# Kernel tuning notes

Measured on AMD Instinct MI355X. Metric: run time of the kernel, lower is better.

## Reference

```python
import jax, jax.numpy as jnp
import numpy as np

B, N, D, H = 2, 2048, 384, 8
Dh = D // H          # 48
G = Dh // 3          # 16 3-vectors per head
EPS = 1e-5


def setup_inputs() -> dict:
    key = jax.random.key(0)
    ks = jax.random.split(key, 8)
    x = jax.random.normal(ks[0], (B, N, D), dtype=jnp.float32)
    # per-node SE(3) frames: proper rotation matrices via QR of random Gaussians
    raw = jax.random.normal(ks[1], (B, N, 3, 3), dtype=jnp.float32)
    q, r = jnp.linalg.qr(raw)
    sign = jnp.sign(jnp.diagonal(r, axis1=-2, axis2=-1))
    frames = q * sign[..., None, :]
    s = 1.0 / np.sqrt(D)
    Wq = jax.random.normal(ks[2], (D, D), dtype=jnp.float32) * s
    Wk = jax.random.normal(ks[3], (D, D), dtype=jnp.float32) * s
    Wv = jax.random.normal(ks[4], (D, D), dtype=jnp.float32) * s
    Wo = jax.random.normal(ks[5], (D, D), dtype=jnp.float32) * s
    bo = jnp.zeros((D,), dtype=jnp.float32)
    gamma = jnp.ones((D,), dtype=jnp.float32)
    beta = jnp.zeros((D,), dtype=jnp.float32)
    return {"x": x, "frames": frames, "Wq": Wq, "Wk": Wk, "Wv": Wv,
            "Wo": Wo, "bo": bo, "gamma": gamma, "beta": beta}


def _rotate(frames, t):
    # t: [B,N,H,Dh] -> rotate each 3-vector chunk by the node's frame R_i
    b, n, h, dh = t.shape
    t3 = t.reshape(b, n, h, dh // 3, 3)
    r3 = jnp.einsum('bnij,bnhgj->bnhgi', frames, t3)
    return r3.reshape(b, n, h, dh)


def reference(x, frames, Wq, Wk, Wv, Wo, bo, gamma, beta):
    b, n, d = x.shape
    Q = (x @ Wq.T).reshape(b, n, H, Dh)
    K = (x @ Wk.T).reshape(b, n, H, Dh)
    V = (x @ Wv.T).reshape(b, n, H, Dh)
    # SE(3) frame-conditioned attention: rotate Q,K into each node's local frame
    Qr = _rotate(frames, Q)
    Kr = _rotate(frames, K)
    scores = jnp.einsum('bqhd,bkhd->bhqk', Qr, Kr) / np.sqrt(Dh)
    attn = jax.nn.softmax(scores, axis=-1)
    out = jnp.einsum('bhqk,bkhd->bqhd', attn, V).reshape(b, n, d)
    out = out @ Wo.T + bo          # out_proj; dropout is identity in eval
    y = x + out                     # residual
    mu = jnp.mean(y, axis=-1, keepdims=True)
    var = jnp.var(y, axis=-1, keepdims=True)
    return (y - mu) * jax.lax.rsqrt(var + EPS) * gamma + beta
```

## Files before the change

### kernel.cpp

```cpp
#include <hip/hip_runtime.h>
#include <hip/hip_bf16.h>
#include <math.h>

constexpr int B = 2, N = 2048, D = 384, H = 8, Dh = 48;
constexpr int M = B * N;
constexpr float EPS = 1e-5f;
constexpr int WSZ = 384 * 384;

typedef short bf16x8 __attribute__((ext_vector_type(8)));
typedef float f32x4 __attribute__((ext_vector_type(4)));

#if __has_builtin(__builtin_amdgcn_exp2f)
#define EXP2(x) __builtin_amdgcn_exp2f(x)
#else
#define EXP2(x) exp2f(x)
#endif

__device__ __forceinline__ ushort f2bf(float f) {
  union { float f; uint u; } v; v.f = f;
  uint r = v.u + 0x7fffu + ((v.u >> 16) & 1u);
  return (ushort)(r >> 16);
}
__device__ __forceinline__ float bf2f(ushort u) {
  union { uint u; float f; } v; v.u = ((uint)u) << 16;
  return v.f;
}
__device__ __forceinline__ uint pk_bf16(float lo, float hi) {
  union { __hip_bfloat162 h; uint u; } v;
  v.h = __float22bfloat162_rn(make_float2(lo, hi));
  return v.u;
}

__device__ __forceinline__ void gload16(const void* g, void* lds) {
  __builtin_amdgcn_global_load_lds(
      (const __attribute__((address_space(1))) unsigned int*)g,
      (__attribute__((address_space(3))) unsigned int*)lds, 16, 0, 0);
}

__global__ __launch_bounds__(256) void pack_all(
    const float* __restrict__ x, const float* __restrict__ Wq,
    const float* __restrict__ Wk, const float* __restrict__ Wv,
    const float* __restrict__ Wo, ushort* __restrict__ xbf,
    ushort* __restrict__ Wqkv, ushort* __restrict__ Wobf) {
  constexpr int XSZ = M * 384;
  int i = (blockIdx.x * 256 + threadIdx.x) * 8;
  const float* src; ushort* dst; int off;
  if (i < XSZ) { src = x; dst = xbf; off = i; }
  else {
    int j = i - XSZ;
    if (j < WSZ)          { src = Wq; dst = Wqkv;           off = j; }
    else if (j < 2 * WSZ) { src = Wk; dst = Wqkv + WSZ;     off = j - WSZ; }
    else if (j < 3 * WSZ) { src = Wv; dst = Wqkv + 2 * WSZ; off = j - 2 * WSZ; }
    else                  { src = Wo; dst = Wobf;           off = j - 3 * WSZ; }
  }
  float4 a = *(const float4*)(src + off);
  float4 b = *(const float4*)(src + off + 4);
  uint4 o;
  o.x = pk_bf16(a.x, a.y);
  o.y = pk_bf16(a.z, a.w);
  o.z = pk_bf16(b.x, b.y);
  o.w = pk_bf16(b.z, b.w);
  *(uint4*)(dst + off) = o;
}

__global__ __launch_bounds__(256) void gemm_qkv(
    const ushort* __restrict__ Abf, const ushort* __restrict__ Wbf,
    ushort* __restrict__ Qpad, ushort* __restrict__ Kpad,
    ushort* __restrict__ Vt) {
  __shared__ ushort Asm[128 * 32];
  __shared__ ushort Bsm[128 * 32];
  const int tid = threadIdx.x, w = tid >> 6, lane = tid & 63;
  const int lq = lane & 15, g = lane >> 4;
  const int brow = blockIdx.y * 128, bcol = blockIdx.x * 128;
  const int wr0 = (w >> 1) * 64, wc0 = (w & 1) * 64;
  const int srow = lane >> 2, scol = (lane & 3) * 8;
  f32x4 acc[4][4];
#pragma unroll
  for (int mi = 0; mi < 4; ++mi)
#pragma unroll
    for (int ni = 0; ni < 4; ++ni) acc[mi][ni] = f32x4{0.f, 0.f, 0.f, 0.f};

  for (int kt = 0; kt < 384; kt += 32) {
    __syncthreads();
#pragma unroll
    for (int i = 0; i < 2; ++i) {
      int seg = w * 2 + i;
      gload16(Abf + (size_t)(brow + seg * 16 + srow) * 384 + kt + scol, Asm + seg * 512);
      gload16(Wbf + (size_t)(bcol + seg * 16 + srow) * 384 + kt + scol, Bsm + seg * 512);
    }
    __syncthreads();
    bf16x8 a[4], b[4];
#pragma unroll
    for (int mi = 0; mi < 4; ++mi)
      a[mi] = *(const bf16x8*)(Asm + (wr0 + mi * 16 + lq) * 32 + g * 8);
#pragma unroll
    for (int ni = 0; ni < 4; ++ni)
      b[ni] = *(const bf16x8*)(Bsm + (wc0 + ni * 16 + lq) * 32 + g * 8);
#pragma unroll
    for (int mi = 0; mi < 4; ++mi)
#pragma unroll
      for (int ni = 0; ni < 4; ++ni)
        acc[mi][ni] = __builtin_amdgcn_mfma_f32_16x16x32_bf16(a[mi], b[ni], acc[mi][ni], 0, 0, 0);
  }

  if (bcol < 768) {
#pragma unroll
    for (int mi = 0; mi < 4; ++mi)
#pragma unroll
      for (int ni = 0; ni < 4; ++ni) {
        int colD = bcol + wc0 + ni * 16 + lq;
        ushort* dstm = (colD < 384) ? Qpad : Kpad;
        int c = (colD < 384) ? colD : colD - 384;
        int hh = c / 48, dh = c - hh * 48;
#pragma unroll
        for (int r = 0; r < 4; ++r) {
          int row = brow + wr0 + mi * 16 + g * 4 + r;
          dstm[(size_t)row * 512 + hh * 64 + dh] = f2bf(acc[mi][ni][r]);
        }
      }
  } else {
#pragma unroll
    for (int mi = 0; mi < 4; ++mi)
#pragma unroll
      for (int ni = 0; ni < 4; ++ni) {
        int vcol = bcol + wc0 + ni * 16 + lq - 768;
        int hh = vcol / 48, dh = vcol - hh * 48;
#pragma unroll
        for (int r = 0; r < 4; ++r) {
          int row = brow + wr0 + mi * 16 + g * 4 + r;
          int bb = row >> 11, nn = row & 2047;
          Vt[((size_t)(bb * H + hh) * 48 + dh) * N + nn] = f2bf(acc[mi][ni][r]);
        }
      }
  }
}

__global__ __launch_bounds__(256) void rotate_both(
    ushort* __restrict__ Q, ushort* __restrict__ K,
    const float* __restrict__ F, float qscale) {
  constexpr int TOT = M * H * 16;
  int idx = blockIdx.x * 256 + threadIdx.x;
  ushort* T = (idx < TOT) ? Q : K;
  float scale = (idx < TOT) ? qscale : 1.0f;
  int rem = (idx < TOT) ? idx : idx - TOT;
  int gq = rem & 15;
  int nh = rem >> 4;
  int h = nh & 7;
  int bn = nh >> 3;
  ushort* p = T + (size_t)bn * 512 + h * 64;
  if (gq < 8) *(uint*)(p + 48 + gq * 2) = 0u;
  ushort* s = p + gq * 3;
  const float* R = F + (size_t)bn * 9;
  float v0 = bf2f(s[0]), v1 = bf2f(s[1]), v2 = bf2f(s[2]);
  float w0 = (R[0] * v0 + R[1] * v1 + R[2] * v2) * scale;
  float w1 = (R[3] * v0 + R[4] * v1 + R[5] * v2) * scale;
  float w2 = (R[6] * v0 + R[7] * v1 + R[8] * v2) * scale;
  s[0] = f2bf(w0); s[1] = f2bf(w1); s[2] = f2bf(w2);
}

__global__ __launch_bounds__(256) void attn_mfma(
    const ushort* __restrict__ Qpad, const ushort* __restrict__ Kpad,
    const ushort* __restrict__ Vt, ushort* __restrict__ Pacc,
    float* __restrict__ Pml) {
  __shared__ ushort K_lds[2][64 * 64];
  __shared__ ushort V_lds[2][48 * 64];
  __shared__ ushort P_lds[4][16 * 64];

  const int bid = blockIdx.x;
  const int wg = (bid & 7) * 128 + (bid >> 3);
  const int qt = wg & 31;
  const int rest = wg >> 5;
  const int h = rest & 7;
  const int b = (rest >> 3) & 1;
  const int half = rest >> 4;
  const int kt0 = half * 1024;
  const int tid = threadIdx.x;
  const int w = tid >> 6;
  const int lane = tid & 63;
  const int lq = lane & 15;
  const int g = lane >> 4;
  const int l7 = lq & 7;
  const int srow8 = lane >> 3;
  const int csw = (lane & 7) ^ srow8;

  const ushort* qp = Qpad + (size_t)(b * N + qt * 64 + w * 16 + lq) * 512 + h * 64;
  bf16x8 qf0 = *(const bf16x8*)(qp + g * 8);
  bf16x8 qf1 = *(const bf16x8*)(qp + 32 + g * 8);

  const ushort* kg0 = Kpad + (size_t)(b * N) * 512 + h * 64
                    + (size_t)(kt0 + w * 8 + srow8) * 512 + csw * 8;
  const ushort* kg1 = kg0 + 32 * 512;
  const ushort* vg0 = Vt + ((size_t)(b * H + h) * 48 + w * 8 + srow8) * (size_t)N
                    + kt0 + csw * 8;
  const ushort* vg1 = vg0 + 32 * (size_t)N;

  auto stage = [&](int buf) {
    gload16(kg0, &K_lds[buf][w * 512]);
    gload16(kg1, &K_lds[buf][(w + 4) * 512]);
    gload16(vg0, &V_lds[buf][w * 512]);
    if (w < 2) gload16(vg1, &V_lds[buf][(w + 4) * 512]);
    kg0 += 64 * 512; kg1 += 64 * 512; vg0 += 64; vg1 += 64;
  };

  float m = -3.0e38f, l = 0.f;
  f32x4 oacc[3];
#pragma unroll
  for (int d = 0; d < 3; ++d) oacc[d] = f32x4{0.f, 0.f, 0.f, 0.f};

  stage(0);
  __syncthreads();
  int cur = 0;

  for (int t = 0; t < 16; ++t) {
    if (t < 15) stage(cur ^ 1);

    const ushort* Kc = K_lds[cur];
    const ushort* Vc = V_lds[cur];

    f32x4 st[4];
#pragma unroll
    for (int t4 = 0; t4 < 4; ++t4) st[t4] = f32x4{0.f, 0.f, 0.f, 0.f};
#pragma unroll
    for (int t4 = 0; t4 < 4; ++t4) {
      int row = t4 * 16 + lq;
      bf16x8 a0 = *(const bf16x8*)(Kc + row * 64 + ((g ^ l7) * 8));
      st[t4] = __builtin_amdgcn_mfma_f32_16x16x32_bf16(a0, qf0, st[t4], 0, 0, 0);
      bf16x8 a1 = *(const bf16x8*)(Kc + row * 64 + (((g ^ 4) ^ l7) * 8));
      st[t4] = __builtin_amdgcn_mfma_f32_16x16x32_bf16(a1, qf1, st[t4], 0, 0, 0);
    }

    float tmax = st[0][0];
#pragma unroll
    for (int t4 = 0; t4 < 4; ++t4)
#pragma unroll
      for (int r = 0; r < 4; ++r) tmax = fmaxf(tmax, st[t4][r]);
    tmax = fmaxf(tmax, __shfl_xor(tmax, 16));
    tmax = fmaxf(tmax, __shfl_xor(tmax, 32));

    if (__ballot(tmax > m + 8.0f)) {
      float mnew = fmaxf(m, tmax);
      float corr = EXP2(m - mnew);
      m = mnew;
      l *= corr;
#pragma unroll
      for (int r = 0; r < 4; ++r) {
        float cr = __shfl(corr, g * 4 + r);
#pragma unroll
        for (int d = 0; d < 3; ++d) oacc[d][r] *= cr;
      }
    }

    float psum = 0.f;
#pragma unroll
    for (int t4 = 0; t4 < 4; ++t4) {
      float p0 = EXP2(st[t4][0] - m);
      float p1 = EXP2(st[t4][1] - m);
      float p2 = EXP2(st[t4][2] - m);
      float p3 = EXP2(st[t4][3] - m);
      psum += (p0 + p1) + (p2 + p3);
      uint2 pk;
      pk.x = pk_bf16(p0, p1);
      pk.y = pk_bf16(p2, p3);
      *(uint2*)(P_lds[w] + lq * 64 + (((2 * t4 + (g >> 1)) ^ l7) * 8) + (g & 1) * 4) = pk;
    }
    psum += __shfl_xor(psum, 16);
    psum += __shfl_xor(psum, 32);
    l += psum;

#pragma unroll
    for (int ks = 0; ks < 2; ++ks) {
      bf16x8 pf = *(const bf16x8*)(P_lds[w] + lq * 64 + ((((ks << 2) | g) ^ l7) * 8));
#pragma unroll
      for (int d = 0; d < 3; ++d) {
        bf16x8 vf = *(const bf16x8*)(Vc + (d * 16 + lq) * 64 + ((((ks << 2) | g) ^ l7) * 8));
        oacc[d] = __builtin_amdgcn_mfma_f32_16x16x32_bf16(pf, vf, oacc[d], 0, 0, 0);
      }
    }

    __syncthreads();
    cur ^= 1;
  }

  const size_t pr0 = ((size_t)((half * B + b) * H + h)) * N + qt * 64 + w * 16;
#pragma unroll
  for (int d = 0; d < 3; ++d)
#pragma unroll
    for (int r = 0; r < 4; ++r)
      Pacc[(pr0 + g * 4 + r) * 48 + d * 16 + lq] = f2bf(oacc[d][r]);
  if (g == 0) {
    Pml[(pr0 + lq) * 2] = m;
    Pml[(pr0 + lq) * 2 + 1] = l;
  }
}

__global__ __launch_bounds__(256) void attn_merge(
    const ushort* __restrict__ Pacc, const float* __restrict__ Pml,
    ushort* __restrict__ Obf) {
  int idx = blockIdx.x * 256 + threadIdx.x;
  int h = idx & 7, bn = idx >> 3;
  int b = bn >> 11, n = bn & 2047;
  size_t r0 = ((size_t)(b * H + h)) * N + n;
  size_t r1 = ((size_t)((B + b) * H + h)) * N + n;
  float m0 = Pml[r0 * 2], l0 = Pml[r0 * 2 + 1];
  float m1 = Pml[r1 * 2], l1 = Pml[r1 * 2 + 1];
  float mm = fmaxf(m0, m1);
  float w0 = EXP2(m0 - mm), w1 = EXP2(m1 - mm);
  float inv = 1.f / (l0 * w0 + l1 * w1);
  w0 *= inv; w1 *= inv;
  const ushort* p0 = Pacc + r0 * 48;
  const ushort* p1 = Pacc + r1 * 48;
  ushort* ob = Obf + (size_t)bn * 384 + h * 48;
#pragma unroll
  for (int j = 0; j < 6; ++j) {
    uint4 a = *(const uint4*)(p0 + j * 8);
    uint4 c = *(const uint4*)(p1 + j * 8);
    uint4 o;
    o.x = pk_bf16(bf2f((ushort)a.x) * w0 + bf2f((ushort)c.x) * w1,
                  bf2f((ushort)(a.x >> 16)) * w0 + bf2f((ushort)(c.x >> 16)) * w1);
    o.y = pk_bf16(bf2f((ushort)a.y) * w0 + bf2f((ushort)c.y) * w1,
                  bf2f((ushort)(a.y >> 16)) * w0 + bf2f((ushort)(c.y >> 16)) * w1);
    o.z = pk_bf16(bf2f((ushort)a.z) * w0 + bf2f((ushort)c.z) * w1,
                  bf2f((ushort)(a.z >> 16)) * w0 + bf2f((ushort)(c.z >> 16)) * w1);
    o.w = pk_bf16(bf2f((ushort)a.w) * w0 + bf2f((ushort)c.w) * w1,
                  bf2f((ushort)(a.w >> 16)) * w0 + bf2f((ushort)(c.w >> 16)) * w1);
    *(uint4*)(ob + j * 8) = o;
  }
}

__global__ __launch_bounds__(256) void gemm_out_ln(
    const ushort* __restrict__ Abf, const ushort* __restrict__ Wbf,
    const float* __restrict__ x, const float* __restrict__ bo,
    const float* __restrict__ gamma, const float* __restrict__ beta,
    float* __restrict__ out) {
  __shared__ ushort Asm[64 * 32];
  __shared__ ushort Bsm[384 * 32];
  const int tid = threadIdx.x, w = tid >> 6, lane = tid & 63;
  const int lq = lane & 15, g = lane >> 4;
  const int brow = blockIdx.x * 64;
  const int srow = lane >> 2, scol = (lane & 3) * 8;
  f32x4 acc[24];
#pragma unroll
  for (int ni = 0; ni < 24; ++ni) acc[ni] = f32x4{0.f, 0.f, 0.f, 0.f};

  for (int kt = 0; kt < 384; kt += 32) {
    __syncthreads();
    gload16(Abf + (size_t)(brow + w * 16 + srow) * 384 + kt + scol, Asm + w * 512);
#pragma unroll
    for (int i = 0; i < 6; ++i) {
      int seg = w * 6 + i;
      gload16(Wbf + (size_t)(seg * 16 + srow) * 384 + kt + scol, Bsm + seg * 512);
    }
    __syncthreads();
    bf16x8 a = *(const bf16x8*)(Asm + (w * 16 + lq) * 32 + g * 8);
#pragma unroll
    for (int ni = 0; ni < 24; ++ni) {
      bf16x8 bfr = *(const bf16x8*)(Bsm + (ni * 16 + lq) * 32 + g * 8);
      acc[ni] = __builtin_amdgcn_mfma_f32_16x16x32_bf16(a, bfr, acc[ni], 0, 0, 0);
    }
  }

  const int row0 = brow + w * 16 + g * 4;
#pragma unroll
  for (int r = 0; r < 4; ++r) {
    const float* xr = x + (size_t)(row0 + r) * 384;
    float s = 0.f, s2 = 0.f;
#pragma unroll
    for (int ni = 0; ni < 24; ++ni) {
      int col = ni * 16 + lq;
      float y = acc[ni][r] + xr[col] + bo[col];
      acc[ni][r] = y;
      s += y; s2 += y * y;
    }
#pragma unroll
    for (int o = 1; o < 16; o <<= 1) {
      s += __shfl_xor(s, o);
      s2 += __shfl_xor(s2, o);
    }
    float mu = s * (1.f / 384.f);
    float var = s2 * (1.f / 384.f) - mu * mu;
    float rstd = rsqrtf(var + EPS);
    float* orow = out + (size_t)(row0 + r) * 384;
#pragma unroll
    for (int ni = 0; ni < 24; ++ni) {
      int col = ni * 16 + lq;
      orow[col] = (acc[ni][r] - mu) * rstd * gamma[col] + beta[col];
    }
  }
}

extern "C" void kernel_launch(void* const* d_in, const int* in_sizes, int n_in,
                              void* d_out, int out_size, void* d_ws, size_t ws_size,
                              hipStream_t stream) {
  const float* x      = (const float*)d_in[0];
  const float* frames = (const float*)d_in[1];
  const float* Wq     = (const float*)d_in[2];
  const float* Wk     = (const float*)d_in[3];
  const float* Wv     = (const float*)d_in[4];
  const float* Wo     = (const float*)d_in[5];
  const float* bo     = (const float*)d_in[6];
  const float* gamma  = (const float*)d_in[7];
  const float* beta   = (const float*)d_in[8];
  float* out = (float*)d_out;

  ushort* xbf  = (ushort*)d_ws;
  ushort* Obf  = xbf;
  ushort* Wqkv = xbf + (size_t)M * 384;
  ushort* Wobf = Wqkv + 3 * (size_t)WSZ;
  ushort* Qpad = Wobf + (size_t)WSZ;
  ushort* Kpad = Qpad + (size_t)M * 512;
  ushort* Vt   = Kpad + (size_t)M * 512;
  ushort* Pacc = Vt + (size_t)M * 384;
  float*  Pml  = (float*)(Pacc + (size_t)2 * B * H * N * 48);

  const float qscale = 0.14433756729740643f * 1.4426950408889634f;

  pack_all<<<(M * 384 + 4 * WSZ) / (8 * 256), 256, 0, stream>>>(
      x, Wq, Wk, Wv, Wo, xbf, Wqkv, Wobf);

  gemm_qkv<<<dim3(9, 32), 256, 0, stream>>>(xbf, Wqkv, Qpad, Kpad, Vt);

  rotate_both<<<2 * M * H * 16 / 256, 256, 0, stream>>>(Qpad, Kpad, frames, qscale);

  attn_mfma<<<2 * B * H * (N / 64), 256, 0, stream>>>(Qpad, Kpad, Vt, Pacc, Pml);

  attn_merge<<<M * H / 256, 256, 0, stream>>>(Pacc, Pml, Obf);

  gemm_out_ln<<<M / 64, 256, 0, stream>>>(Obf, Wobf, x, bo, gamma, beta, out);
}
```

Baseline: 86.45 us.

## Retile QKV and out-proj GEMMs, make attention waves own two query tiles

The QKV GEMM drops from 128-row to 64-row tiles, doubling the grid. The output-projection+LayerNorm GEMM uses 16-row blocks with columns split across waves and a shared-memory row reduction, giving four times as many blocks. Attention runs 128-thread blocks where each wave handles two 16-row query tiles, reusing each K/V fragment twice. The P matrix now stays in registers, relying on the permuted K row layout, instead of round-tripping through LDS. These trade larger per-thread register state and extra reduction syncs for more parallelism and less LDS traffic.

```diff
diff --git a/kernel.cpp b/kernel.cpp
--- a/kernel.cpp
+++ b/kernel.cpp
@@ -67,37 +67,37 @@
     const ushort* __restrict__ Abf, const ushort* __restrict__ Wbf,
     ushort* __restrict__ Qpad, ushort* __restrict__ Kpad,
     ushort* __restrict__ Vt) {
-  __shared__ ushort Asm[128 * 32];
+  __shared__ ushort Asm[64 * 32];
   __shared__ ushort Bsm[128 * 32];
   const int tid = threadIdx.x, w = tid >> 6, lane = tid & 63;
   const int lq = lane & 15, g = lane >> 4;
-  const int brow = blockIdx.y * 128, bcol = blockIdx.x * 128;
-  const int wr0 = (w >> 1) * 64, wc0 = (w & 1) * 64;
+  const int brow = blockIdx.y * 64, bcol = blockIdx.x * 128;
+  const int wr0 = (w >> 1) * 32, wc0 = (w & 1) * 64;
   const int srow = lane >> 2, scol = (lane & 3) * 8;
-  f32x4 acc[4][4];
-#pragma unroll
-  for (int mi = 0; mi < 4; ++mi)
+  f32x4 acc[2][4];
+#pragma unroll
+  for (int mi = 0; mi < 2; ++mi)
 #pragma unroll
     for (int ni = 0; ni < 4; ++ni) acc[mi][ni] = f32x4{0.f, 0.f, 0.f, 0.f};
 
   for (int kt = 0; kt < 384; kt += 32) {
     __syncthreads();
+    gload16(Abf + (size_t)(brow + w * 16 + srow) * 384 + kt + scol, Asm + w * 512);
 #pragma unroll
     for (int i = 0; i < 2; ++i) {
       int seg = w * 2 + i;
-      gload16(Abf + (size_t)(brow + seg * 16 + srow) * 384 + kt + scol, Asm + seg * 512);
       gload16(Wbf + (size_t)(bcol + seg * 16 + srow) * 384 + kt + scol, Bsm + seg * 512);
     }
     __syncthreads();
-    bf16x8 a[4], b[4];
-#pragma unroll
-    for (int mi = 0; mi < 4; ++mi)
+    bf16x8 a[2], b[4];
+#pragma unroll
+    for (int mi = 0; mi < 2; ++mi)
       a[mi] = *(const bf16x8*)(Asm + (wr0 + mi * 16 + lq) * 32 + g * 8);
 #pragma unroll
     for (int ni = 0; ni < 4; ++ni)
       b[ni] = *(const bf16x8*)(Bsm + (wc0 + ni * 16 + lq) * 32 + g * 8);
 #pragma unroll
-    for (int mi = 0; mi < 4; ++mi)
+    for (int mi = 0; mi < 2; ++mi)
 #pragma unroll
       for (int ni = 0; ni < 4; ++ni)
         acc[mi][ni] = __builtin_amdgcn_mfma_f32_16x16x32_bf16(a[mi], b[ni], acc[mi][ni], 0, 0, 0);
@@ -105,7 +105,7 @@
 
   if (bcol < 768) {
 #pragma unroll
-    for (int mi = 0; mi < 4; ++mi)
+    for (int mi = 0; mi < 2; ++mi)
 #pragma unroll
       for (int ni = 0; ni < 4; ++ni) {
         int colD = bcol + wc0 + ni * 16 + lq;
@@ -120,7 +120,7 @@
       }
   } else {
 #pragma unroll
-    for (int mi = 0; mi < 4; ++mi)
+    for (int mi = 0; mi < 2; ++mi)
 #pragma unroll
       for (int ni = 0; ni < 4; ++ni) {
         int vcol = bcol + wc0 + ni * 16 + lq - 768;
@@ -158,13 +158,15 @@
   s[0] = f2bf(w0); s[1] = f2bf(w1); s[2] = f2bf(w2);
 }
 
-__global__ __launch_bounds__(256) void attn_mfma(
+__global__ __launch_bounds__(128) void attn_mfma(
     const ushort* __restrict__ Qpad, const ushort* __restrict__ Kpad,
     const ushort* __restrict__ Vt, ushort* __restrict__ Pacc,
     float* __restrict__ Pml) {
-  __shared__ ushort K_lds[2][64 * 64];
-  __shared__ ushort V_lds[2][48 * 64];
-  __shared__ ushort P_lds[4][16 * 64];
+  __shared__ __align__(16) ushort SH[14336];
+  ushort* K0 = SH;
+  ushort* K1 = SH + 4096;
+  ushort* V0 = SH + 8192;
+  ushort* V1 = SH + 11264;
 
   const int bid = blockIdx.x;
   const int wg = (bid & 7) * 128 + (bid >> 3);
@@ -181,115 +183,167 @@
   const int g = lane >> 4;
   const int l7 = lq & 7;
   const int srow8 = lane >> 3;
-  const int csw = (lane & 7) ^ srow8;
-
-  const ushort* qp = Qpad + (size_t)(b * N + qt * 64 + w * 16 + lq) * 512 + h * 64;
-  bf16x8 qf0 = *(const bf16x8*)(qp + g * 8);
-  bf16x8 qf1 = *(const bf16x8*)(qp + 32 + g * 8);
-
-  const ushort* kg0 = Kpad + (size_t)(b * N) * 512 + h * 64
-                    + (size_t)(kt0 + w * 8 + srow8) * 512 + csw * 8;
-  const ushort* kg1 = kg0 + 32 * 512;
-  const ushort* vg0 = Vt + ((size_t)(b * H + h) * 48 + w * 8 + srow8) * (size_t)N
-                    + kt0 + csw * 8;
-  const ushort* vg1 = vg0 + 32 * (size_t)N;
-
-  auto stage = [&](int buf) {
-    gload16(kg0, &K_lds[buf][w * 512]);
-    gload16(kg1, &K_lds[buf][(w + 4) * 512]);
-    gload16(vg0, &V_lds[buf][w * 512]);
-    if (w < 2) gload16(vg1, &V_lds[buf][(w + 4) * 512]);
-    kg0 += 64 * 512; kg1 += 64 * 512; vg0 += 64; vg1 += 64;
+  const int c8 = (lane & 7) ^ srow8;
+
+  bf16x8 qf[2][2];
+  {
+    const ushort* qb = Qpad + ((size_t)(b * N) + qt * 64 + w * 32) * 512 + h * 64;
+#pragma unroll
+    for (int i = 0; i < 2; ++i)
+#pragma unroll
+      for (int kd = 0; kd < 2; ++kd)
+        qf[i][kd] = *(const bf16x8*)(qb + (size_t)(i * 16 + lq) * 512 + kd * 32 + g * 8);
+  }
+
+  const ushort* kg[4];
+#pragma unroll
+  for (int j = 0; j < 4; ++j) {
+    int s = w + 2 * j;
+    int kappa = (s >> 2) * 32 + (s & 1) * 16 + (srow8 >> 2) * 8 + ((s >> 1) & 1) * 4 + (srow8 & 3);
+    kg[j] = Kpad + ((size_t)(b * N) + kt0 + kappa) * 512 + h * 64 + c8 * 8;
+  }
+  const ushort* vg[3];
+#pragma unroll
+  for (int j = 0; j < 3; ++j) {
+    int sv = w + 2 * j;
+    vg[j] = Vt + ((size_t)(b * H + h) * 48 + sv * 8 + srow8) * (size_t)N + kt0 + c8 * 8;
+  }
+
+  auto stage = [&](ushort* kb, ushort* vb) {
+#pragma unroll
+    for (int j = 0; j < 4; ++j) {
+      gload16(kg[j], kb + (w + 2 * j) * 512);
+      kg[j] += 64 * 512;
+    }
+#pragma unroll
+    for (int j = 0; j < 3; ++j) {
+      gload16(vg[j], vb + (w + 2 * j) * 512);
+      vg[j] += 64;
+    }
   };
 
-  float m = -3.0e38f, l = 0.f;
-  f32x4 oacc[3];
-#pragma unroll
-  for (int d = 0; d < 3; ++d) oacc[d] = f32x4{0.f, 0.f, 0.f, 0.f};
-
-  stage(0);
+  float m[2] = {-3.0e38f, -3.0e38f}, l[2] = {0.f, 0.f};
+  f32x4 oacc[2][3];
+#pragma unroll
+  for (int i = 0; i < 2; ++i)
+#pragma unroll
+    for (int d = 0; d < 3; ++d) oacc[i][d] = f32x4{0.f, 0.f, 0.f, 0.f};
+
+  stage(K0, V0);
   __syncthreads();
   int cur = 0;
 
   for (int t = 0; t < 16; ++t) {
-    if (t < 15) stage(cur ^ 1);
-
-    const ushort* Kc = K_lds[cur];
-    const ushort* Vc = V_lds[cur];
-
-    f32x4 st[4];
-#pragma unroll
-    for (int t4 = 0; t4 < 4; ++t4) st[t4] = f32x4{0.f, 0.f, 0.f, 0.f};
+    if (t < 15) stage(cur ? K0 : K1, cur ? V0 : V1);
+    const ushort* Kc = cur ? K1 : K0;
+    const ushort* Vc = cur ? V1 : V0;
+
+    f32x4 st[2][4];
+#pragma unroll
+    for (int i = 0; i < 2; ++i)
+#pragma unroll
+      for (int t4 = 0; t4 < 4; ++t4) st[i][t4] = f32x4{0.f, 0.f, 0.f, 0.f};
 #pragma unroll
     for (int t4 = 0; t4 < 4; ++t4) {
-      int row = t4 * 16 + lq;
-      bf16x8 a0 = *(const bf16x8*)(Kc + row * 64 + ((g ^ l7) * 8));
-      st[t4] = __builtin_amdgcn_mfma_f32_16x16x32_bf16(a0, qf0, st[t4], 0, 0, 0);
-      bf16x8 a1 = *(const bf16x8*)(Kc + row * 64 + (((g ^ 4) ^ l7) * 8));
-      st[t4] = __builtin_amdgcn_mfma_f32_16x16x32_bf16(a1, qf1, st[t4], 0, 0, 0);
-    }
-
-    float tmax = st[0][0];
-#pragma unroll
-    for (int t4 = 0; t4 < 4; ++t4)
-#pragma unroll
-      for (int r = 0; r < 4; ++r) tmax = fmaxf(tmax, st[t4][r]);
-    tmax = fmaxf(tmax, __shfl_xor(tmax, 16));
-    tmax = fmaxf(tmax, __shfl_xor(tmax, 32));
-
-    if (__ballot(tmax > m + 8.0f)) {
-      float mnew = fmaxf(m, tmax);
-      float corr = EXP2(m - mnew);
-      m = mnew;
-      l *= corr;
-#pragma unroll
-      for (int r = 0; r < 4; ++r) {
-        float cr = __shfl(corr, g * 4 + r);
-#pragma unroll
-        for (int d = 0; d < 3; ++d) oacc[d][r] *= cr;
+      bf16x8 a0 = *(const bf16x8*)(Kc + (t4 * 16 + lq) * 64 + ((g ^ l7) * 8));
+      bf16x8 a1 = *(const bf16x8*)(Kc + (t4 * 16 + lq) * 64 + (((g + 4) ^ l7) * 8));
+#pragma unroll
+      for (int i = 0; i < 2; ++i) {
+        st[i][t4] = __builtin_amdgcn_mfma_f32_16x16x32_bf16(a0, qf[i][0], st[i][t4], 0, 0, 0);
+        st[i][t4] = __builtin_amdgcn_mfma_f32_16x16x32_bf16(a1, qf[i][1], st[i][t4], 0, 0, 0);
       }
     }
 
-    float psum = 0.f;
-#pragma unroll
-    for (int t4 = 0; t4 < 4; ++t4) {
-      float p0 = EXP2(st[t4][0] - m);
-      float p1 = EXP2(st[t4][1] - m);
-      float p2 = EXP2(st[t4][2] - m);
-      float p3 = EXP2(st[t4][3] - m);
-      psum += (p0 + p1) + (p2 + p3);
-      uint2 pk;
-      pk.x = pk_bf16(p0, p1);
-      pk.y = pk_bf16(p2, p3);
-      *(uint2*)(P_lds[w] + lq * 64 + (((2 * t4 + (g >> 1)) ^ l7) * 8) + (g & 1) * 4) = pk;
-    }
-    psum += __shfl_xor(psum, 16);
-    psum += __shfl_xor(psum, 32);
-    l += psum;
-
-#pragma unroll
-    for (int ks = 0; ks < 2; ++ks) {
-      bf16x8 pf = *(const bf16x8*)(P_lds[w] + lq * 64 + ((((ks << 2) | g) ^ l7) * 8));
-#pragma unroll
-      for (int d = 0; d < 3; ++d) {
-        bf16x8 vf = *(const bf16x8*)(Vc + (d * 16 + lq) * 64 + ((((ks << 2) | g) ^ l7) * 8));
-        oacc[d] = __builtin_amdgcn_mfma_f32_16x16x32_bf16(pf, vf, oacc[d], 0, 0, 0);
+    bf16x8 vf[2][3];
+#pragma unroll
+    for (int ks = 0; ks < 2; ++ks)
+#pragma unroll
+      for (int d = 0; d < 3; ++d)
+        vf[ks][d] = *(const bf16x8*)(Vc + (d * 16 + lq) * 64 + ((((ks << 2) | g) ^ l7) * 8));
+
+    float tmax[2];
+#pragma unroll
+    for (int i = 0; i < 2; ++i) {
+      float t0 = st[i][0][0];
+#pragma unroll
+      for (int t4 = 0; t4 < 4; ++t4)
+#pragma unroll
+        for (int r = 0; r < 4; ++r) t0 = fmaxf(t0, st[i][t4][r]);
+      t0 = fmaxf(t0, __shfl_xor(t0, 16));
+      t0 = fmaxf(t0, __shfl_xor(t0, 32));
+      tmax[i] = t0;
+    }
+    bool need = (tmax[0] > m[0] + 8.0f) | (tmax[1] > m[1] + 8.0f);
+    if (__ballot(need)) {
+#pragma unroll
+      for (int i = 0; i < 2; ++i) {
+        float mnew = fmaxf(m[i], tmax[i]);
+        float corr = EXP2(m[i] - mnew);
+        m[i] = mnew;
+        l[i] *= corr;
+#pragma unroll
+        for (int r = 0; r < 4; ++r) {
+          float cr = __shfl(corr, g * 4 + r);
+#pragma unroll
+          for (int d = 0; d < 3; ++d) oacc[i][d][r] *= cr;
+        }
       }
     }
+
+    bf16x8 pf[2][2];
+#pragma unroll
+    for (int i = 0; i < 2; ++i) {
+      float ps = 0.f;
+      uint u0[4], u1[4];
+#pragma unroll
+      for (int t4 = 0; t4 < 4; ++t4) {
+        float p0 = EXP2(st[i][t4][0] - m[i]);
+        float p1 = EXP2(st[i][t4][1] - m[i]);
+        float p2 = EXP2(st[i][t4][2] - m[i]);
+        float p3 = EXP2(st[i][t4][3] - m[i]);
+        ps += (p0 + p1) + (p2 + p3);
+        if (t4 < 2) {
+          u0[(t4 & 1) * 2]     = pk_bf16(p0, p1);
+          u0[(t4 & 1) * 2 + 1] = pk_bf16(p2, p3);
+        } else {
+          u1[(t4 & 1) * 2]     = pk_bf16(p0, p1);
+          u1[(t4 & 1) * 2 + 1] = pk_bf16(p2, p3);
+        }
+      }
+      ps += __shfl_xor(ps, 16);
+      ps += __shfl_xor(ps, 32);
+      l[i] += ps;
+      union { uint4 q; bf16x8 v; } c0, c1;
+      c0.q = make_uint4(u0[0], u0[1], u0[2], u0[3]);
+      c1.q = make_uint4(u1[0], u1[1], u1[2], u1[3]);
+      pf[i][0] = c0.v;
+      pf[i][1] = c1.v;
+    }
+
+#pragma unroll
+    for (int ks = 0; ks < 2; ++ks)
+#pragma unroll
+      for (int i = 0; i < 2; ++i)
+#pragma unroll
+        for (int d = 0; d < 3; ++d)
+          oacc[i][d] = __builtin_amdgcn_mfma_f32_16x16x32_bf16(pf[i][ks], vf[ks][d], oacc[i][d], 0, 0, 0);
 
     __syncthreads();
     cur ^= 1;
   }
 
-  const size_t pr0 = ((size_t)((half * B + b) * H + h)) * N + qt * 64 + w * 16;
-#pragma unroll
-  for (int d = 0; d < 3; ++d)
-#pragma unroll
-    for (int r = 0; r < 4; ++r)
-      Pacc[(pr0 + g * 4 + r) * 48 + d * 16 + lq] = f2bf(oacc[d][r]);
-  if (g == 0) {
-    Pml[(pr0 + lq) * 2] = m;
-    Pml[(pr0 + lq) * 2 + 1] = l;
+#pragma unroll
+  for (int i = 0; i < 2; ++i) {
+    const size_t pr0 = ((size_t)((half * B + b) * H + h)) * N + qt * 64 + (w * 2 + i) * 16;
+#pragma unroll
+    for (int d = 0; d < 3; ++d)
+#pragma unroll
+      for (int r = 0; r < 4; ++r)
+        Pacc[(pr0 + g * 4 + r) * 48 + d * 16 + lq] = f2bf(oacc[i][d][r]);
+    if (g == 0) {
+      Pml[(pr0 + lq) * 2] = m[i];
+      Pml[(pr0 + lq) * 2 + 1] = l[i];
+    }
   }
 }
 
@@ -332,57 +386,74 @@
     const float* __restrict__ x, const float* __restrict__ bo,
     const float* __restrict__ gamma, const float* __restrict__ beta,
     float* __restrict__ out) {
-  __shared__ ushort Asm[64 * 32];
+  __shared__ ushort Asm[16 * 32];
   __shared__ ushort Bsm[384 * 32];
+  __shared__ float red[4][16][2];
   const int tid = threadIdx.x, w = tid >> 6, lane = tid & 63;
   const int lq = lane & 15, g = lane >> 4;
-  const int brow = blockIdx.x * 64;
+  const int brow = blockIdx.x * 16;
   const int srow = lane >> 2, scol = (lane & 3) * 8;
-  f32x4 acc[24];
-#pragma unroll
-  for (int ni = 0; ni < 24; ++ni) acc[ni] = f32x4{0.f, 0.f, 0.f, 0.f};
+  f32x4 acc[6];
+#pragma unroll
+  for (int ni = 0; ni < 6; ++ni) acc[ni] = f32x4{0.f, 0.f, 0.f, 0.f};
 
   for (int kt = 0; kt < 384; kt += 32) {
     __syncthreads();
-    gload16(Abf + (size_t)(brow + w * 16 + srow) * 384 + kt + scol, Asm + w * 512);
+    if (w == 0) gload16(Abf + (size_t)(brow + srow) * 384 + kt + scol, Asm);
 #pragma unroll
     for (int i = 0; i < 6; ++i) {
       int seg = w * 6 + i;
       gload16(Wbf + (size_t)(seg * 16 + srow) * 384 + kt + scol, Bsm + seg * 512);
     }
     __syncthreads();
-    bf16x8 a = *(const bf16x8*)(Asm + (w * 16 + lq) * 32 + g * 8);
-#pragma unroll
-    for (int ni = 0; ni < 24; ++ni) {
-      bf16x8 bfr = *(const bf16x8*)(Bsm + (ni * 16 + lq) * 32 + g * 8);
-      acc[ni] = __builtin_amdgcn_mfma_f32_16x16x32_bf16(a, bfr, acc[ni], 0, 0, 0);
-    }
-  }
-
-  const int row0 = brow + w * 16 + g * 4;
+    bf16x8 a = *(const bf16x8*)(Asm + lq * 32 + g * 8);
+#pragma unroll
+    for (int ni = 0; ni < 6; ++ni) {
+      bf16x8 bb = *(const bf16x8*)(Bsm + ((w * 6 + ni) * 16 + lq) * 32 + g * 8);
+      acc[ni] = __builtin_amdgcn_mfma_f32_16x16x32_bf16(a, bb, acc[ni], 0, 0, 0);
+    }
+  }
+
+  float s[4] = {0.f, 0.f, 0.f, 0.f}, s2[4] = {0.f, 0.f, 0.f, 0.f};
+#pragma unroll
+  for (int ni = 0; ni < 6; ++ni) {
+    int col = (w * 6 + ni) * 16 + lq;
+    float bcol = bo[col];
+#pragma unroll
+    for (int r = 0; r < 4; ++r) {
+      float y = acc[ni][r] + x[(size_t)(brow + g * 4 + r) * 384 + col] + bcol;
+      acc[ni][r] = y;
+      s[r] += y; s2[r] += y * y;
+    }
+  }
+#pragma unroll
+  for (int o = 1; o < 16; o <<= 1) {
+#pragma unroll
+    for (int r = 0; r < 4; ++r) {
+      s[r] += __shfl_xor(s[r], o);
+      s2[r] += __shfl_xor(s2[r], o);
+    }
+  }
+  if (lq == 0) {
+#pragma unroll
+    for (int r = 0; r < 4; ++r) {
+      red[w][g * 4 + r][0] = s[r];
+      red[w][g * 4 + r][1] = s2[r];
+    }
+  }
+  __syncthreads();
 #pragma unroll
   for (int r = 0; r < 4; ++r) {
-    const float* xr = x + (size_t)(row0 + r) * 384;
-    float s = 0.f, s2 = 0.f;
-#pragma unroll
-    for (int ni = 0; ni < 24; ++ni) {
-      int col = ni * 16 + lq;
-      float y = acc[ni][r] + xr[col] + bo[col];
-      acc[ni][r] = y;
-      s += y; s2 += y * y;
-    }
-#pragma unroll
-    for (int o = 1; o < 16; o <<= 1) {
-      s += __shfl_xor(s, o);
-      s2 += __shfl_xor(s2, o);
-    }
-    float mu = s * (1.f / 384.f);
-    float var = s2 * (1.f / 384.f) - mu * mu;
+    int row = g * 4 + r;
+    float ts  = red[0][row][0] + red[1][row][0] + red[2][row][0] + red[3][row][0];
+    float ts2 = red[0][row][1] + red[1][row][1] + red[2][row][1] + red[3][row][1];
+    float mu = ts * (1.f / 384.f);
+    float var = ts2 * (1.f / 384.f) - mu * mu;
     float rstd = rsqrtf(var + EPS);
-    float* orow = out + (size_t)(row0 + r) * 384;
-#pragma unroll
-    for (int ni = 0; ni < 24; ++ni) {
-      int col = ni * 16 + lq;
+    float* orow = out + (size_t)(brow + row) * 384;
+#pragma unroll
+    for (int ni = 0; ni < 6; ++ni) {
+      int col = (w * 6 + ni) * 16 + lq;
       orow[col] = (acc[ni][r] - mu) * rstd * gamma[col] + beta[col];
     }
   }
@@ -417,13 +488,13 @@
   pack_all<<<(M * 384 + 4 * WSZ) / (8 * 256), 256, 0, stream>>>(
       x, Wq, Wk, Wv, Wo, xbf, Wqkv, Wobf);
 
-  gemm_qkv<<<dim3(9, 32), 256, 0, stream>>>(xbf, Wqkv, Qpad, Kpad, Vt);
+  gemm_qkv<<<dim3(9, 64), 256, 0, stream>>>(xbf, Wqkv, Qpad, Kpad, Vt);
 
   rotate_both<<<2 * M * H * 16 / 256, 256, 0, stream>>>(Qpad, Kpad, frames, qscale);
 
-  attn_mfma<<<2 * B * H * (N / 64), 256, 0, stream>>>(Qpad, Kpad, Vt, Pacc, Pml);
+  attn_mfma<<<2 * B * H * (N / 64), 128, 0, stream>>>(Qpad, Kpad, Vt, Pacc, Pml);
 
   attn_merge<<<M * H / 256, 256, 0, stream>>>(Pacc, Pml, Obf);
 
-  gemm_out_ln<<<M / 64, 256, 0, stream>>>(Obf, Wobf, x, bo, gamma, beta, out);
-}
+  gemm_out_ln<<<M / 16, 256, 0, stream>>>(Obf, Wobf, x, bo, gamma, beta, out);
+}
```

Measured after the change: 78.42 us. 1.1x faster.
